# Optimization experiments

Hardware: AMD Instinct MI355X
Metric: run time of the kernel (lower is better)

The kernel has to match this reference:

```python
import jax, jax.numpy as jnp
import numpy as np

B, KPLUS1, D = 64, 513, 1024

def setup_inputs() -> dict:
    key = jax.random.key(0)
    k1, k2, k3 = jax.random.split(key, 3)
    x = jax.random.normal(k1, (B, KPLUS1, D), dtype=jnp.float32)
    # glorot-style scaled init for faithfulness in magnitude
    dense_weights = jax.random.normal(k2, (2 * D, D), dtype=jnp.float32) * (1.0 / np.sqrt(2 * D))
    dot_bias = jax.random.normal(k3, (D, 1), dtype=jnp.float32) * (1.0 / np.sqrt(D))
    return {"x": x, "dense_weights": dense_weights, "dot_bias": dot_bias}

def reference(x, dense_weights, dot_bias):
    # x: [B, K+1, D]; x[:,0] = sentence encoding u, x[:,1:] = knowledge z_t
    u = x[:, 0, :]            # [B, D]
    z = x[:, 1:, :]           # [B, K, D]
    d = z.shape[-1]
    # concat(z_t, u) @ W1 == z @ W1[:D] + u @ W1[D:], broadcast over K
    # (mathematically identical to the tile+concat+matmul in the original)
    w_z = dense_weights[:d, :]   # [D, D]
    w_u = dense_weights[d:, :]   # [D, D]
    m = jnp.tanh(jnp.einsum('bkd,de->bke', z, w_z)
                 + jnp.einsum('bd,de->be', u, w_u)[:, None, :])  # [B, K, D]
    q = jnp.einsum('bke,e->bk', m, dot_bias[:, 0])               # [B, K]
    return jax.nn.softmax(q, axis=-1)                            # [B, K]
```

## Files before the change

kernel.cpp:

```cpp
#include <hip/hip_runtime.h>
#include <hip/hip_bf16.h>


typedef __attribute__((ext_vector_type(8))) short short8;
typedef __attribute__((ext_vector_type(8))) _Float16 half8;
typedef __attribute__((ext_vector_type(4))) float f32x4;
typedef unsigned short ushort_t;

typedef const __attribute__((address_space(1))) void gvoid_t;
typedef __attribute__((address_space(3))) void lvoid_t;

__device__ __forceinline__ ushort_t f2bf(float f) {
    unsigned u = __float_as_uint(f);
    unsigned r = u + 0x7FFFu + ((u >> 16) & 1u);
    return (ushort_t)(r >> 16);
}
__device__ __forceinline__ float bf2f(ushort_t h) {
    return __uint_as_float(((unsigned)h) << 16);
}
__device__ __forceinline__ float tanh_fast(float x) {
    float e = __expf(2.f * x);
    return 1.f - 2.f / (e + 1.f);
}

__global__ void k_prep_w16(const float* __restrict__ w,
                           _Float16* __restrict__ wzt) {
    __shared__ _Float16 th[64][66];
    const int k0 = blockIdx.x * 64;
    const int n0 = blockIdx.y * 64;
    const int t = threadIdx.x;
    const int lr = t >> 6;
    const int lc = t & 63;
#pragma unroll
    for (int r = 0; r < 16; ++r) {
        int kk = r * 4 + lr;
        th[kk][lc] = (_Float16)w[(size_t)(k0 + kk) * 1024 + n0 + lc];
    }
    __syncthreads();
#pragma unroll
    for (int r = 0; r < 16; ++r) {
        int nn = r * 4 + lr;
        wzt[(size_t)(n0 + nn) * 1024 + k0 + lc] = th[lc][nn];
    }
}

__global__ void k_hu(const float* __restrict__ x,
                     const float* __restrict__ w,
                     float* __restrict__ hu) {
    __shared__ float us[1024];
    const int b = blockIdx.y;
    const int e = blockIdx.x * 256 + threadIdx.x;
    for (int i = threadIdx.x; i < 1024; i += 256)
        us[i] = x[(size_t)b * 513 * 1024 + i];
    __syncthreads();
    const float* wu = w + (size_t)1024 * 1024;
    float acc = 0.f;
#pragma unroll 8
    for (int d = 0; d < 1024; ++d)
        acc = fmaf(us[d], wu[(size_t)d * 1024 + e], acc);
    hu[b * 1024 + e] = acc;
}

__global__ __launch_bounds__(512, 2) void k_gemm10(
        const float* __restrict__ x,
        const _Float16* __restrict__ wzt,
        const float* __restrict__ hu,
        const float* __restrict__ bias,
        float* __restrict__ qp) {
    __shared__ __align__(16) _Float16 As[256 * 64];
    __shared__ __align__(16) _Float16 Bs[256 * 64];
    __shared__ float qred[2][4][128];

    const int t = threadIdx.x;
    const int mtile = blockIdx.x;
    const int ntile = blockIdx.y;
    const int wid = t >> 6;
    const int l = t & 63;
    const int wm = wid >> 2;
    const int wn = wid & 3;
    const int lr = l & 15;
    const int g = l >> 4;

    const int srow = t >> 3;
    const int sphys = (t & 7) ^ (srow & 7);
    const int schunk = sphys;
    const int bb = mtile >> 1;
    size_t aSrc[4];
#pragma unroll
    for (int j = 0; j < 4; ++j) {
        int m = mtile * 256 + srow + j * 64;
        int kk = m & 511;
        aSrc[j] = ((size_t)(bb * 513 + 1 + kk) << 10) + (t & 7) * 8;
    }
    int aDst[4];
#pragma unroll
    for (int j = 0; j < 4; ++j)
        aDst[j] = (srow + j * 64) * 128 + sphys * 16;
    size_t bSrc[4];
#pragma unroll
    for (int j = 0; j < 4; ++j)
        bSrc[j] = (size_t)(ntile * 256 + srow + j * 64) * 1024 + schunk * 8;
    const int bDst0 = t * 16;

    f32x4 acc[8][4] = {};

    for (int k0 = 0; k0 < 1024; k0 += 64) {
#pragma unroll
        for (int j = 0; j < 4; ++j) {
            __builtin_amdgcn_global_load_lds(
                (gvoid_t*)(wzt + bSrc[j] + k0),
                (lvoid_t*)((char*)Bs + j * 8192 + bDst0), 16, 0, 0);
        }
#pragma unroll
        for (int j = 0; j < 4; ++j) {
            const float4 v0 = *(const float4*)(x + aSrc[j] + k0);
            const float4 v1 = *(const float4*)(x + aSrc[j] + k0 + 4);
            half8 hv;
            hv[0] = (_Float16)v0.x; hv[1] = (_Float16)v0.y;
            hv[2] = (_Float16)v0.z; hv[3] = (_Float16)v0.w;
            hv[4] = (_Float16)v1.x; hv[5] = (_Float16)v1.y;
            hv[6] = (_Float16)v1.z; hv[7] = (_Float16)v1.w;
            *(half8*)((char*)As + aDst[j]) = hv;
        }
        __syncthreads();

#pragma unroll
        for (int ks = 0; ks < 2; ++ks) {
            half8 afr[8], bfr[4];
            const int so = ((ks * 4 + g) ^ (lr & 7)) * 16;
#pragma unroll
            for (int ni = 0; ni < 4; ++ni)
                bfr[ni] = *(const half8*)((const char*)Bs + (wn * 64 + ni * 16 + lr) * 128 + so);
#pragma unroll
            for (int mi = 0; mi < 8; ++mi)
                afr[mi] = *(const half8*)((const char*)As + (wm * 128 + mi * 16 + lr) * 128 + so);
#pragma unroll
            for (int mi = 0; mi < 8; ++mi)
#pragma unroll
                for (int ni = 0; ni < 4; ++ni)
                    acc[mi][ni] = __builtin_amdgcn_mfma_f32_16x16x32_f16(
                        afr[mi], bfr[ni], acc[mi][ni], 0, 0, 0);
        }
        __syncthreads();
    }

    float hu4[4], bias4[4];
#pragma unroll
    for (int ni = 0; ni < 4; ++ni) {
        int e = ntile * 256 + wn * 64 + ni * 16 + lr;
        hu4[ni] = hu[bb * 1024 + e];
        bias4[ni] = bias[e];
    }
#pragma unroll
    for (int mi = 0; mi < 8; ++mi) {
#pragma unroll
        for (int j = 0; j < 4; ++j) {
            float v = 0.f;
#pragma unroll
            for (int ni = 0; ni < 4; ++ni)
                v += tanh_fast(acc[mi][ni][j] + hu4[ni]) * bias4[ni];
            v += __shfl_xor(v, 1);
            v += __shfl_xor(v, 2);
            v += __shfl_xor(v, 4);
            v += __shfl_xor(v, 8);
            if (lr == 0)
                qred[wm][wn][mi * 16 + g * 4 + j] = v;
        }
    }
    __syncthreads();
    if (t < 256) {
        const int wmr = t >> 7;
        const int rr = t & 127;
        float q = qred[wmr][0][rr] + qred[wmr][1][rr]
                + qred[wmr][2][rr] + qred[wmr][3][rr];
        qp[(size_t)ntile * 32768 + mtile * 256 + t] = q;
    }
}

__global__ void k_prep_w(const float* __restrict__ w,
                         ushort_t* __restrict__ wzt_hi,
                         ushort_t* __restrict__ wzt_lo) {
    __shared__ ushort_t th[64][66];
    __shared__ ushort_t tl[64][66];
    const int k0 = blockIdx.x * 64;
    const int n0 = blockIdx.y * 64;
    const int t = threadIdx.x;
    const int lr = t >> 6;
    const int lc = t & 63;
#pragma unroll
    for (int r = 0; r < 16; ++r) {
        int kk = r * 4 + lr;
        float f = w[(size_t)(k0 + kk) * 1024 + n0 + lc];
        ushort_t hi = f2bf(f);
        ushort_t lo = f2bf(f - bf2f(hi));
        th[kk][lc] = hi;
        tl[kk][lc] = lo;
    }
    __syncthreads();
#pragma unroll
    for (int r = 0; r < 16; ++r) {
        int nn = r * 4 + lr;
        wzt_hi[(size_t)(n0 + nn) * 1024 + k0 + lc] = th[lc][nn];
        wzt_lo[(size_t)(n0 + nn) * 1024 + k0 + lc] = tl[lc][nn];
    }
}

__global__ __launch_bounds__(256) void k_gemm(
        const float* __restrict__ x,
        const ushort_t* __restrict__ wzt_hi,
        const ushort_t* __restrict__ wzt_lo,
        const float* __restrict__ hu,
        const float* __restrict__ bias,
        float* __restrict__ qp) {
    __shared__ ushort_t As_hi[128][40];
    __shared__ ushort_t As_lo[128][40];
    __shared__ ushort_t Bs_hi[128][40];
    __shared__ ushort_t Bs_lo[128][40];
    __shared__ float qred[2][2][64];

    const int t = threadIdx.x;
    const int mtile = blockIdx.x;
    const int ntile = blockIdx.y;
    const int wid = t >> 6;
    const int l = t & 63;
    const int wm = wid >> 1;
    const int wn = wid & 1;

    f32x4 acc[4][4] = {};

    const int arow = t >> 3;
    const int acol = (t & 7) * 4;
    size_t abase[4];
#pragma unroll
    for (int it = 0; it < 4; ++it) {
        int m = mtile * 128 + arow + it * 32;
        int bb = m >> 9;
        int kk = m & 511;
        abase[it] = ((size_t)(bb * 513 + 1 + kk)) * 1024 + acol;
    }
    const int brow = t >> 2;
    const int bcol = (t & 3) * 8;
    const size_t bbase = (size_t)(ntile * 128 + brow) * 1024 + bcol;

    for (int k0 = 0; k0 < 1024; k0 += 32) {
#pragma unroll
        for (int it = 0; it < 4; ++it) {
            const float4 v = *(const float4*)(x + abase[it] + k0);
            ushort4 hv, lv;
            hv.x = f2bf(v.x); lv.x = f2bf(v.x - bf2f(hv.x));
            hv.y = f2bf(v.y); lv.y = f2bf(v.y - bf2f(hv.y));
            hv.z = f2bf(v.z); lv.z = f2bf(v.z - bf2f(hv.z));
            hv.w = f2bf(v.w); lv.w = f2bf(v.w - bf2f(hv.w));
            const int row = arow + it * 32;
            *(ushort4*)&As_hi[row][acol] = hv;
            *(ushort4*)&As_lo[row][acol] = lv;
        }
#pragma unroll
        for (int it = 0; it < 2; ++it) {
            const int row = brow + it * 64;
            const uint4 vh = *(const uint4*)(wzt_hi + bbase + (size_t)it * 64 * 1024 + k0);
            const uint4 vl = *(const uint4*)(wzt_lo + bbase + (size_t)it * 64 * 1024 + k0);
            *(uint4*)&Bs_hi[row][bcol] = vh;
            *(uint4*)&Bs_lo[row][bcol] = vl;
        }
        __syncthreads();

        const int lr = l & 15;
        const int lk = (l >> 4) * 8;
        short8 ah[4], al[4], bh[4], bl[4];
#pragma unroll
        for (int i = 0; i < 4; ++i) {
            ah[i] = *(const short8*)&As_hi[wm * 64 + i * 16 + lr][lk];
            al[i] = *(const short8*)&As_lo[wm * 64 + i * 16 + lr][lk];
            bh[i] = *(const short8*)&Bs_hi[wn * 64 + i * 16 + lr][lk];
            bl[i] = *(const short8*)&Bs_lo[wn * 64 + i * 16 + lr][lk];
        }
#pragma unroll
        for (int mi = 0; mi < 4; ++mi)
#pragma unroll
            for (int ni = 0; ni < 4; ++ni) {
                acc[mi][ni] = __builtin_amdgcn_mfma_f32_16x16x32_bf16(ah[mi], bh[ni], acc[mi][ni], 0, 0, 0);
                acc[mi][ni] = __builtin_amdgcn_mfma_f32_16x16x32_bf16(ah[mi], bl[ni], acc[mi][ni], 0, 0, 0);
                acc[mi][ni] = __builtin_amdgcn_mfma_f32_16x16x32_bf16(al[mi], bh[ni], acc[mi][ni], 0, 0, 0);
            }
        __syncthreads();
    }

    const int lr = l & 15;
    const int lg = l >> 4;
    const int bbatch = mtile >> 2;
    float hu4[4], bias4[4];
#pragma unroll
    for (int ni = 0; ni < 4; ++ni) {
        int e = ntile * 128 + wn * 64 + ni * 16 + lr;
        hu4[ni] = hu[bbatch * 1024 + e];
        bias4[ni] = bias[e];
    }
#pragma unroll
    for (int mi = 0; mi < 4; ++mi) {
#pragma unroll
        for (int j = 0; j < 4; ++j) {
            float v = 0.f;
#pragma unroll
            for (int ni = 0; ni < 4; ++ni)
                v += tanhf(acc[mi][ni][j] + hu4[ni]) * bias4[ni];
            v += __shfl_xor(v, 1);
            v += __shfl_xor(v, 2);
            v += __shfl_xor(v, 4);
            v += __shfl_xor(v, 8);
            if (lr == 0)
                qred[wm][wn][mi * 16 + lg * 4 + j] = v;
        }
    }
    __syncthreads();
    if (t < 128) {
        const int wmr = t >> 6;
        const int rr = t & 63;
        float qv = qred[wmr][0][rr] + qred[wmr][1][rr];
        qp[(size_t)ntile * 32768 + mtile * 128 + t] = qv;
    }
}

__global__ void k_softmax(const float* __restrict__ qp, float* __restrict__ out,
                          int nt) {
    const int b = blockIdx.x;
    const int k = threadIdx.x;
    float q = 0.f;
    for (int i = 0; i < nt; ++i)
        q += qp[(size_t)i * 32768 + b * 512 + k];

    __shared__ float redm[8];
    __shared__ float reds[8];
    const int wid = k >> 6;

    float m = q;
#pragma unroll
    for (int off = 32; off >= 1; off >>= 1)
        m = fmaxf(m, __shfl_xor(m, off));
    if ((k & 63) == 0) redm[wid] = m;
    __syncthreads();
    m = redm[0];
#pragma unroll
    for (int i = 1; i < 8; ++i) m = fmaxf(m, redm[i]);

    float p = expf(q - m);
    float s = p;
#pragma unroll
    for (int off = 32; off >= 1; off >>= 1)
        s += __shfl_xor(s, off);
    if ((k & 63) == 0) reds[wid] = s;
    __syncthreads();
    s = 0.f;
#pragma unroll
    for (int i = 0; i < 8; ++i) s += reds[i];

    out[b * 512 + k] = p / s;
}

extern "C" void kernel_launch(void* const* d_in, const int* in_sizes, int n_in,
                              void* d_out, int out_size, void* d_ws, size_t ws_size,
                              hipStream_t stream) {
    const float* x    = (const float*)d_in[0];
    const float* w    = (const float*)d_in[1];
    const float* bias = (const float*)d_in[2];
    float* out = (float*)d_out;

    char* ws = (char*)d_ws;

    const size_t need = (size_t)1024 * 1024 * sizeof(_Float16)
                      + (size_t)64 * 1024 * sizeof(float)
                      + (size_t)4 * 32768 * sizeof(float);

    if (ws_size >= need) {
        _Float16* wzt = (_Float16*)ws;
        float*    hu  = (float*)(wzt + (size_t)1024 * 1024);
        float*    qp  = hu + (size_t)64 * 1024;

        k_prep_w16<<<dim3(16, 16), 256, 0, stream>>>(w, wzt);
        k_hu<<<dim3(4, 64), 256, 0, stream>>>(x, w, hu);
        k_gemm10<<<dim3(128, 4), 512, 0, stream>>>(x, wzt, hu, bias, qp);
        k_softmax<<<64, 512, 0, stream>>>(qp, out, 4);
    } else {
        ushort_t* wzt_hi = (ushort_t*)ws;
        ushort_t* wzt_lo = wzt_hi + (size_t)1024 * 1024;
        float* hu = (float*)(ws + (size_t)4 * 1024 * 1024);
        float* qp = hu + (size_t)64 * 1024;

        k_prep_w<<<dim3(16, 16), 256, 0, stream>>>(w, wzt_hi, wzt_lo);
        k_hu<<<dim3(4, 64), 256, 0, stream>>>(x, w, hu);
        k_gemm<<<dim3(256, 8), 256, 0, stream>>>(x, wzt_hi, wzt_lo, hu, bias, qp);
        k_softmax<<<64, 512, 0, stream>>>(qp, out, 8);
    }
}
```

Before: 174.2 us.

## Double-buffer the LDS tiles and prefetch A into registers in the fp16 GEMM

The fp16 GEMM moves to two LDS stages. While the current tile is computed, the next B tile is loaded straight into the other buffer and the next A tile is loaded into registers, then converted and written at the start of the following iteration. Hand-placed waitcnt, barrier and sched_barrier calls order the stages, and s_setprio raises wave priority around the MFMA block. The aim is to hide global-load latency behind MFMA work. In exchange, each block now uses about 132KB of LDS, which probably allows only one 512-thread block per CU instead of two.

```diff
diff --git a/kernel.cpp b/kernel.cpp
--- a/kernel.cpp
+++ b/kernel.cpp
@@ -61,14 +61,13 @@
     hu[b * 1024 + e] = acc;
 }
 
-__global__ __launch_bounds__(512, 2) void k_gemm10(
+__global__ __launch_bounds__(512, 2) void k_gemm11(
         const float* __restrict__ x,
         const _Float16* __restrict__ wzt,
         const float* __restrict__ hu,
         const float* __restrict__ bias,
         float* __restrict__ qp) {
-    __shared__ __align__(16) _Float16 As[256 * 64];
-    __shared__ __align__(16) _Float16 Bs[256 * 64];
+    __shared__ __align__(16) char lds[2 * 65536];
     __shared__ float qred[2][4][128];
 
     const int t = threadIdx.x;
@@ -83,66 +82,119 @@
 
     const int srow = t >> 3;
     const int sphys = (t & 7) ^ (srow & 7);
-    const int schunk = sphys;
     const int bb = mtile >> 1;
     size_t aSrc[4];
+    int aDst[4];
+    size_t bSrc[4];
 #pragma unroll
     for (int j = 0; j < 4; ++j) {
         int m = mtile * 256 + srow + j * 64;
         int kk = m & 511;
         aSrc[j] = ((size_t)(bb * 513 + 1 + kk) << 10) + (t & 7) * 8;
-    }
-    int aDst[4];
-#pragma unroll
-    for (int j = 0; j < 4; ++j)
         aDst[j] = (srow + j * 64) * 128 + sphys * 16;
-    size_t bSrc[4];
-#pragma unroll
-    for (int j = 0; j < 4; ++j)
-        bSrc[j] = (size_t)(ntile * 256 + srow + j * 64) * 1024 + schunk * 8;
-    const int bDst0 = t * 16;
+        bSrc[j] = (size_t)(ntile * 256 + srow + j * 64) * 1024 + sphys * 8;
+    }
+    const int bDst0 = 32768 + t * 16;
 
     f32x4 acc[8][4] = {};
-
-    for (int k0 = 0; k0 < 1024; k0 += 64) {
-#pragma unroll
-        for (int j = 0; j < 4; ++j) {
-            __builtin_amdgcn_global_load_lds(
-                (gvoid_t*)(wzt + bSrc[j] + k0),
-                (lvoid_t*)((char*)Bs + j * 8192 + bDst0), 16, 0, 0);
-        }
-#pragma unroll
-        for (int j = 0; j < 4; ++j) {
-            const float4 v0 = *(const float4*)(x + aSrc[j] + k0);
-            const float4 v1 = *(const float4*)(x + aSrc[j] + k0 + 4);
-            half8 hv;
-            hv[0] = (_Float16)v0.x; hv[1] = (_Float16)v0.y;
-            hv[2] = (_Float16)v0.z; hv[3] = (_Float16)v0.w;
-            hv[4] = (_Float16)v1.x; hv[5] = (_Float16)v1.y;
-            hv[6] = (_Float16)v1.z; hv[7] = (_Float16)v1.w;
-            *(half8*)((char*)As + aDst[j]) = hv;
-        }
-        __syncthreads();
-
-#pragma unroll
-        for (int ks = 0; ks < 2; ++ks) {
-            half8 afr[8], bfr[4];
-            const int so = ((ks * 4 + g) ^ (lr & 7)) * 16;
-#pragma unroll
-            for (int ni = 0; ni < 4; ++ni)
-                bfr[ni] = *(const half8*)((const char*)Bs + (wn * 64 + ni * 16 + lr) * 128 + so);
-#pragma unroll
-            for (int mi = 0; mi < 8; ++mi)
-                afr[mi] = *(const half8*)((const char*)As + (wm * 128 + mi * 16 + lr) * 128 + so);
-#pragma unroll
-            for (int mi = 0; mi < 8; ++mi)
-#pragma unroll
-                for (int ni = 0; ni < 4; ++ni)
-                    acc[mi][ni] = __builtin_amdgcn_mfma_f32_16x16x32_f16(
-                        afr[mi], bfr[ni], acc[mi][ni], 0, 0, 0);
-        }
-        __syncthreads();
-    }
+    float4 pa0_, pa1_, pa2_, pa3_, pb0_, pb1_, pb2_, pb3_;
+
+#define A_LOAD(k0)                                                           \
+    {   pa0_ = *(const float4*)(x + aSrc[0] + (k0));                         \
+        pb0_ = *(const float4*)(x + aSrc[0] + (k0) + 4);                     \
+        pa1_ = *(const float4*)(x + aSrc[1] + (k0));                         \
+        pb1_ = *(const float4*)(x + aSrc[1] + (k0) + 4);                     \
+        pa2_ = *(const float4*)(x + aSrc[2] + (k0));                         \
+        pb2_ = *(const float4*)(x + aSrc[2] + (k0) + 4);                     \
+        pa3_ = *(const float4*)(x + aSrc[3] + (k0));                         \
+        pb3_ = *(const float4*)(x + aSrc[3] + (k0) + 4); }
+
+#define B_STAGE(k0, BUF)                                                     \
+    {   _Pragma("unroll")                                                    \
+        for (int j = 0; j < 4; ++j)                                          \
+            __builtin_amdgcn_global_load_lds(                                \
+                (gvoid_t*)(wzt + bSrc[j] + (k0)),                            \
+                (lvoid_t*)((BUF) + bDst0 + j * 8192), 16, 0, 0); }
+
+#define A_CVT_WRITE(BUF)                                                     \
+    {   half8 hv;                                                            \
+        hv[0] = (_Float16)pa0_.x; hv[1] = (_Float16)pa0_.y;                  \
+        hv[2] = (_Float16)pa0_.z; hv[3] = (_Float16)pa0_.w;                  \
+        hv[4] = (_Float16)pb0_.x; hv[5] = (_Float16)pb0_.y;                  \
+        hv[6] = (_Float16)pb0_.z; hv[7] = (_Float16)pb0_.w;                  \
+        *(half8*)((BUF) + aDst[0]) = hv;                                     \
+        hv[0] = (_Float16)pa1_.x; hv[1] = (_Float16)pa1_.y;                  \
+        hv[2] = (_Float16)pa1_.z; hv[3] = (_Float16)pa1_.w;                  \
+        hv[4] = (_Float16)pb1_.x; hv[5] = (_Float16)pb1_.y;                  \
+        hv[6] = (_Float16)pb1_.z; hv[7] = (_Float16)pb1_.w;                  \
+        *(half8*)((BUF) + aDst[1]) = hv;                                     \
+        hv[0] = (_Float16)pa2_.x; hv[1] = (_Float16)pa2_.y;                  \
+        hv[2] = (_Float16)pa2_.z; hv[3] = (_Float16)pa2_.w;                  \
+        hv[4] = (_Float16)pb2_.x; hv[5] = (_Float16)pb2_.y;                  \
+        hv[6] = (_Float16)pb2_.z; hv[7] = (_Float16)pb2_.w;                  \
+        *(half8*)((BUF) + aDst[2]) = hv;                                     \
+        hv[0] = (_Float16)pa3_.x; hv[1] = (_Float16)pa3_.y;                  \
+        hv[2] = (_Float16)pa3_.z; hv[3] = (_Float16)pa3_.w;                  \
+        hv[4] = (_Float16)pb3_.x; hv[5] = (_Float16)pb3_.y;                  \
+        hv[6] = (_Float16)pb3_.z; hv[7] = (_Float16)pb3_.w;                  \
+        *(half8*)((BUF) + aDst[3]) = hv; }
+
+#define COMPUTE(BUF)                                                         \
+    {   _Pragma("unroll")                                                    \
+        for (int ks = 0; ks < 2; ++ks) {                                     \
+            half8 afr[8], bfr[4];                                            \
+            const int so = ((ks * 4 + g) ^ (lr & 7)) * 16;                   \
+            _Pragma("unroll")                                                \
+            for (int ni = 0; ni < 4; ++ni)                                   \
+                bfr[ni] = *(const half8*)((BUF) + 32768                      \
+                          + (wn * 64 + ni * 16 + lr) * 128 + so);            \
+            _Pragma("unroll")                                                \
+            for (int mi = 0; mi < 8; ++mi)                                   \
+                afr[mi] = *(const half8*)((BUF)                              \
+                          + (wm * 128 + mi * 16 + lr) * 128 + so);           \
+            __builtin_amdgcn_s_setprio(1);                                   \
+            _Pragma("unroll")                                                \
+            for (int mi = 0; mi < 8; ++mi)                                   \
+                _Pragma("unroll")                                            \
+                for (int ni = 0; ni < 4; ++ni)                               \
+                    acc[mi][ni] = __builtin_amdgcn_mfma_f32_16x16x32_f16(    \
+                        afr[mi], bfr[ni], acc[mi][ni], 0, 0, 0);             \
+            __builtin_amdgcn_s_setprio(0);                                   \
+        } }
+
+    A_LOAD(0)
+    B_STAGE(0, lds)
+
+#pragma unroll 1
+    for (int T = 0; T < 15; ++T) {
+        char* buf = lds + (T & 1) * 65536;
+        char* nbuf = lds + ((T + 1) & 1) * 65536;
+        const int k1 = (T + 1) * 64;
+        A_CVT_WRITE(buf)
+        A_LOAD(k1)
+        B_STAGE(k1, nbuf)
+        asm volatile("s_waitcnt lgkmcnt(0)" ::: "memory");
+        asm volatile("s_waitcnt vmcnt(12)" ::: "memory");
+        __builtin_amdgcn_sched_barrier(0);
+        __builtin_amdgcn_s_barrier();
+        COMPUTE(buf)
+        __builtin_amdgcn_s_barrier();
+        __builtin_amdgcn_sched_barrier(0);
+    }
+    {
+        char* buf = lds + (15 & 1) * 65536;
+        A_CVT_WRITE(buf)
+        asm volatile("s_waitcnt lgkmcnt(0)" ::: "memory");
+        asm volatile("s_waitcnt vmcnt(0)" ::: "memory");
+        __builtin_amdgcn_sched_barrier(0);
+        __builtin_amdgcn_s_barrier();
+        COMPUTE(buf)
+        __builtin_amdgcn_s_barrier();
+    }
+#undef COMPUTE
+#undef A_CVT_WRITE
+#undef B_STAGE
+#undef A_LOAD
 
     float hu4[4], bias4[4];
 #pragma unroll
@@ -378,7 +430,7 @@
 
         k_prep_w16<<<dim3(16, 16), 256, 0, stream>>>(w, wzt);
         k_hu<<<dim3(4, 64), 256, 0, stream>>>(x, w, hu);
-        k_gemm10<<<dim3(128, 4), 512, 0, stream>>>(x, wzt, hu, bias, qp);
+        k_gemm11<<<dim3(128, 4), 512, 0, stream>>>(x, wzt, hu, bias, qp);
         k_softmax<<<64, 512, 0, stream>>>(qp, out, 4);
     } else {
         ushort_t* wzt_hi = (ushort_t*)ws;
```

Measured after the change: 173.3 us. About the same (-0.5%).
